# Performance work log

Hardware: AMD Instinct MI355X
Metric: run time of the kernel (lower is better)

## Reference

```python
import jax, jax.numpy as jnp
import numpy as np

B, T, D = 4, 8160, 1024
N, H = 8, 128            # heads, units_per_head (D == N*H)
W = 12                   # block_size
LEFT_CTX = 13            # atten_left_context
L = LEFT_CTX - 1         # left context frames beyond current position
R = 0                    # atten_right_context
C = W + L + R            # context_size = 24
CAP = 50.0               # attention_logits_soft_capping


def _timing_signal(pos, channels):
    # sinusoidal embedding, channels even (1024)
    pos = pos.astype(jnp.float32)
    nt = channels // 2
    inc = np.log(10000.0) / max(nt - 1, 1)
    inv = jnp.exp(jnp.arange(nt, dtype=jnp.float32) * -inc)
    st = pos[:, :, None] * inv[None, None, :]
    return jnp.concatenate([jnp.sin(st), jnp.cos(st)], axis=2)


def _extract_block_context(x, block_size, left, right, pad_val):
    # x: [B, T, ...] -> [B, num_blocks, context_size, ...]
    pads = [(0, 0)] * x.ndim
    pads[1] = (left, right + block_size - 1)
    xp = jnp.pad(x, pads, constant_values=jnp.asarray(pad_val, x.dtype))
    frame_len = block_size + left + right
    num_frames = (xp.shape[1] - frame_len) // block_size + 1
    idx = jnp.arange(num_frames)[:, None] * block_size + jnp.arange(frame_len)[None, :]
    return jnp.take(xp, idx, axis=1)


def _convert_to_block(x, block_size):
    b, t = x.shape[0], x.shape[1]
    nb = t // block_size  # T chosen as multiple of block_size
    return x.reshape((b, nb, block_size) + x.shape[2:])


def setup_inputs() -> dict:
    key = jax.random.key(0)
    ks = jax.random.split(key, 6)
    x = jax.random.normal(ks[0], (B, T, D), dtype=jnp.float32)
    mask = jnp.ones((B, T), dtype=bool)
    i = jnp.arange(W)[:, None]
    j = jnp.arange(C)[None, :]
    causal_valid_mask = (j >= i) & (j - i <= L + R)  # [W, C]
    s = 1.0 / np.sqrt(D)
    wq = jax.random.normal(ks[1], (D, D), dtype=jnp.float32) * s
    wk = jax.random.normal(ks[2], (D, D), dtype=jnp.float32) * s
    wv = jax.random.normal(ks[3], (D, D), dtype=jnp.float32) * s
    pos_proj = jax.random.normal(ks[4], (D, N, H), dtype=jnp.float32) * s
    return {"x": x, "mask": mask, "causal_valid_mask": causal_valid_mask,
            "wq": wq, "wk": wk, "wv": wv, "pos_proj": pos_proj}


def reference(x, mask, causal_valid_mask, wq, wk, wv, pos_proj):
    b, t, d = x.shape
    u = t // W
    q = jnp.einsum('btd,df->btf', x, wq).reshape(b, t, N, H)
    k = jnp.einsum('btd,df->btf', x, wk).reshape(b, t, N, H)
    v = jnp.einsum('btd,df->btf', x, wv).reshape(b, t, N, H)

    q_blk = _convert_to_block(q, W) * (H ** -0.5)        # [B,U,W,N,H]
    k_ctx = _extract_block_context(k, W, L, R, 0.0)      # [B,U,C,N,H]
    v_ctx = _extract_block_context(v, W, L, R, 0.0)      # [B,U,C,N,H]

    # term A+C: content logits
    term_ac = jnp.einsum('BuwNH,BucNH->BNuwc', q_blk, k_ctx)

    # term B+D: relative position logits via skew trick
    pos = jnp.arange(L, -R - 1, -1)[None, :]             # [1, L+R+1]
    sin_emb = _timing_signal(pos, D)                     # [1, L+R+1, D]
    sin_emb = jnp.einsum('fd,dnh->fnh', sin_emb[0], pos_proj)  # [F,N,H]
    term_bd = jnp.einsum('BuwNH,FNH->BNuwF', q_blk, sin_emb)   # [B,N,U,W,F]
    term_bd = jnp.pad(term_bd, ((0, 0),) * 4 + ((0, C + 1 - (L + R + 1)),))
    term_bd = term_bd.reshape(b, N, u, W * (C + 1))[:, :, :, :W * C]
    term_bd = term_bd.reshape(b, N, u, W, C)

    logits = term_ac + term_bd
    logits = CAP * jnp.tanh(logits / CAP)

    mask_ctx = _extract_block_context(mask, W, L, R, False)    # [B,U,C]
    valid = mask_ctx[:, None, :, None, :] & causal_valid_mask[None, None, None, :, :]
    logits = jnp.where(valid, logits, jnp.asarray(-1e9, logits.dtype))
    probs = jax.nn.softmax(logits, axis=-1)              # [B,N,U,W,C]

    out = jnp.einsum('BNuwc,BucNH->BuwNH', probs, v_ctx)
    return out.reshape(b, u * W, N, H)[:, :t]            # [B,T,N,H]
```

## Files before the change

### kernel.cpp

```cpp
#include <hip/hip_runtime.h>
#include <cstdint>
#include <cstddef>


typedef __bf16 bf16_t;
typedef float  floatx4 __attribute__((ext_vector_type(4)));
typedef __bf16 bf16x8  __attribute__((ext_vector_type(8)));
typedef __bf16 bf16x4  __attribute__((ext_vector_type(4)));

#define GLDS16(gp, lp)                                                        \
  __builtin_amdgcn_global_load_lds(                                           \
      (const __attribute__((address_space(1))) void*)(gp),                    \
      (__attribute__((address_space(3))) void*)(lp), 16, 0, 0)

static constexpr int kT     = 8160;
static constexpr int kM     = 4 * kT;
static constexpr int kU     = kT / 12;
static constexpr int kNC    = 3200;
static constexpr size_t kArrE = (size_t)4 * 8 * 8160 * 128;

__global__ __launch_bounds__(256) void convert_x(const float* __restrict__ X,
                                                 bf16_t* __restrict__ Xb) {
  const size_t i = ((size_t)blockIdx.x * 256 + threadIdx.x) * 8;
  float4 a = *(const float4*)(X + i);
  float4 b = *(const float4*)(X + i + 4);
  bf16x8 o;
  o[0] = (bf16_t)a.x; o[1] = (bf16_t)a.y; o[2] = (bf16_t)a.z; o[3] = (bf16_t)a.w;
  o[4] = (bf16_t)b.x; o[5] = (bf16_t)b.y; o[6] = (bf16_t)b.z; o[7] = (bf16_t)b.w;
  *(bf16x8*)(Xb + i) = o;
}

__global__ __launch_bounds__(512) void posemb_k(const float* __restrict__ pp,
                                                float* __restrict__ pe) {
  __shared__ float st[1024];
  __shared__ float red[4][128];
  const int d   = blockIdx.x;
  const int fc  = blockIdx.y;
  const int tid = threadIdx.x;
  const float dpos = (float)d;
  for (int i = tid; i < 1024; i += 512) {
    int idx = i & 511;
    float freq = expf(-(float)idx * (9.2103403719761836f / 511.0f));
    float a = dpos * freq;
    st[i] = (i < 512) ? sinf(a) : cosf(a);
  }
  __syncthreads();
  const int part = tid >> 7;
  const int fl   = tid & 127;
  const int f    = fc * 128 + fl;
  float acc = 0.f;
  const int dd0 = part * 256;
#pragma unroll 8
  for (int dd = dd0; dd < dd0 + 256; ++dd)
    acc += st[dd] * pp[(size_t)dd * 1024 + f];
  red[part][fl] = acc;
  __syncthreads();
  if (tid < 128)
    pe[(size_t)d * 1024 + f] = red[0][fl] + red[1][fl] + red[2][fl] + red[3][fl];
}

__global__ __launch_bounds__(256) void transpose_w(const float* __restrict__ Wq,
                                                   const float* __restrict__ Wk,
                                                   const float* __restrict__ Wv,
                                                   bf16_t* __restrict__ Wt) {
  __shared__ float tile[64][65];
  const int g = blockIdx.z;
  const float* W = (g == 0) ? Wq : (g == 1) ? Wk : Wv;
  bf16_t* O = Wt + (size_t)g * 1024 * 1024;
  const int k0 = blockIdx.x * 64, n0 = blockIdx.y * 64;
  const int col = threadIdx.x & 63, r4 = threadIdx.x >> 6;
#pragma unroll
  for (int i = 0; i < 16; ++i) {
    int row = i * 4 + r4;
    tile[row][col] = W[(size_t)(k0 + row) * 1024 + n0 + col];
  }
  __syncthreads();
#pragma unroll
  for (int i = 0; i < 16; ++i) {
    int row = i * 4 + r4;
    O[(size_t)(n0 + row) * 1024 + k0 + col] = (bf16_t)tile[col][row];
  }
}

__global__ __launch_bounds__(256) void pe2w(const float* __restrict__ pe,
                                            bf16_t* __restrict__ Wt) {
  const int idx = blockIdx.x;
  const int tid = threadIdx.x;
  bf16_t* out = Wt + (size_t)(3072 + idx) * 1024;
  if (idx >= 104) {
    bf16x4 z = {};
    *(bf16x4*)(out + tid * 4) = z;
    return;
  }
  const int n = idx / 13, d = idx - n * 13;
  __shared__ float peh[128];
  if (tid < 128) peh[tid] = pe[(size_t)d * 1024 + n * 128 + tid];
  __syncthreads();
  float acc[4] = {};
  const bf16_t* wb = Wt + (size_t)(n * 128) * 1024 + tid * 4;
#pragma unroll 8
  for (int h = 0; h < 128; ++h) {
    bf16x4 w4 = *(const bf16x4*)(wb + (size_t)h * 1024);
    float s = peh[h];
    acc[0] += s * (float)w4[0];
    acc[1] += s * (float)w4[1];
    acc[2] += s * (float)w4[2];
    acc[3] += s * (float)w4[3];
  }
  bf16x4 o;
  o[0] = (bf16_t)acc[0]; o[1] = (bf16_t)acc[1];
  o[2] = (bf16_t)acc[2]; o[3] = (bf16_t)acc[3];
  *(bf16x4*)(out + tid * 4) = o;
}

__global__ __launch_bounds__(512, 2) void qkv_gemm(const bf16_t* __restrict__ X,
                                                   const bf16_t* __restrict__ Wt,
                                                   bf16_t* __restrict__ O) {
  __shared__ __align__(16) bf16_t lds[8][8192];

  const int flat = blockIdx.x;
  const int work = (flat & 7) * 208 + (flat >> 3);
  const int mt = work / 13, nt = work % 13;
  const int m0 = mt * 256, n0 = nt * 256;

  const int tid  = threadIdx.x;
  const int wave = tid >> 6;
  const int lane = tid & 63;
  const int wm   = wave >> 2;
  const int wn   = wave & 3;
  const int qd   = lane >> 4;
  const int lr   = lane & 15;

  const int rr  = tid >> 3;
  const int cg8 = ((tid & 7) ^ (rr & 7)) * 8;
  const bf16_t* aP[4];
  const bf16_t* bP[4];
  {
    int r2 = m0 + 128 + rr, r3 = m0 + 192 + rr;
    aP[0] = X + (size_t)(m0 + rr) * 1024 + cg8;
    aP[1] = X + (size_t)(m0 + 64 + rr) * 1024 + cg8;
    aP[2] = X + (size_t)(r2 < kM ? r2 : 0) * 1024 + cg8;
    aP[3] = X + (size_t)(r3 < kM ? r3 : 0) * 1024 + cg8;
    int s2 = n0 + 128 + rr, s3 = n0 + 192 + rr;
    bP[0] = Wt + (size_t)(n0 + rr) * 1024 + cg8;
    bP[1] = Wt + (size_t)(n0 + 64 + rr) * 1024 + cg8;
    bP[2] = Wt + (size_t)(s2 < kNC ? s2 : 0) * 1024 + cg8;
    bP[3] = Wt + (size_t)(s3 < kNC ? s3 : 0) * 1024 + cg8;
  }

#define STAGE_A(h, t)                                                          \
  do {                                                                         \
    bf16_t* d_ = &lds[((t) & 1) * 4 + (h)][wave * 512];                        \
    GLDS16(aP[2 * (h)]     + (size_t)(t) * 64, d_);                            \
    GLDS16(aP[2 * (h) + 1] + (size_t)(t) * 64, d_ + 4096);                     \
  } while (0)
#define STAGE_B(h, t)                                                          \
  do {                                                                         \
    bf16_t* d_ = &lds[((t) & 1) * 4 + 2 + (h)][wave * 512];                    \
    GLDS16(bP[2 * (h)]     + (size_t)(t) * 64, d_);                            \
    GLDS16(bP[2 * (h) + 1] + (size_t)(t) * 64, d_ + 4096);                     \
  } while (0)

  auto frag = [&](int slot, int r, int cb) -> bf16x8 {
    uint32_t off = (uint32_t)(r * 128 + cb) ^ (uint32_t)((r & 7) << 4);
    return *(const bf16x8*)((const char*)&lds[slot][0] + off);
  };

  floatx4 acc[8][4] = {};

  STAGE_A(0, 0); STAGE_A(1, 0); STAGE_B(0, 0); STAGE_B(1, 0);
  STAGE_B(0, 1); STAGE_B(1, 1);
  asm volatile("s_waitcnt vmcnt(4)" ::: "memory");
  __builtin_amdgcn_s_barrier();

  const int aslot0 = wm;
  const int bslot0 = 2 + (wn >> 1);
  const int brow0  = (wn & 1) * 64;

#pragma unroll 2
  for (int t = 0; t < 16; ++t) {
    const int par = (t & 1) * 4;
    bf16x8 bfrag[4][2];
#pragma unroll
    for (int p = 0; p < 4; ++p) {
      if (p == 0) {
#pragma unroll
        for (int in = 0; in < 4; ++in)
#pragma unroll
          for (int k2 = 0; k2 < 2; ++k2)
            bfrag[in][k2] =
                frag(par + bslot0, brow0 + in * 16 + lr, k2 * 64 + qd * 16);
      }
      bf16x8 afrag[2][2];
#pragma unroll
      for (int i = 0; i < 2; ++i)
#pragma unroll
        for (int k2 = 0; k2 < 2; ++k2)
          afrag[i][k2] =
              frag(par + aslot0, (2 * p + i) * 16 + lr, k2 * 64 + qd * 16);

      if (p == 0)      { if (t < 15) STAGE_A(0, t + 1); }
      else if (p == 1) { if (t < 15) STAGE_A(1, t + 1); }
      else if (p == 2) { if (t < 14) STAGE_B(0, t + 2); }
      else             { if (t < 14) STAGE_B(1, t + 2); }

      if (p == 3) {
        if (t < 14) asm volatile("s_waitcnt vmcnt(4)" ::: "memory");
        else        asm volatile("s_waitcnt vmcnt(0)" ::: "memory");
      }
      __builtin_amdgcn_s_barrier();
      asm volatile("s_waitcnt lgkmcnt(0)" ::: "memory");
      __builtin_amdgcn_sched_barrier(0);

      __builtin_amdgcn_s_setprio(1);
#pragma unroll
      for (int i = 0; i < 2; ++i)
#pragma unroll
        for (int in = 0; in < 4; ++in)
#pragma unroll
          for (int k2 = 0; k2 < 2; ++k2)
            acc[2 * p + i][in] = __builtin_amdgcn_mfma_f32_16x16x32_bf16(
                afrag[i][k2], bfrag[in][k2], acc[2 * p + i][in], 0, 0, 0);
      __builtin_amdgcn_s_setprio(0);
      __builtin_amdgcn_sched_barrier(0);
      __builtin_amdgcn_s_barrier();
    }
  }
#undef STAGE_A
#undef STAGE_B

  const int mBase = m0 + wm * 128 + qd * 4;
  const int nBase = n0 + wn * 64 + lr;
  bf16_t* QPE = O + 3 * kArrE;
  if (n0 < 3072) {
    const bool interior = (m0 + 256 <= kM);
#pragma unroll
    for (int im = 0; im < 8; ++im)
#pragma unroll
      for (int r = 0; r < 4; ++r) {
        const int mm = mBase + im * 16 + r;
        if (!interior && mm >= kM) continue;
        const int bb = mm / 8160;
        const int tt = mm - bb * 8160;
#pragma unroll
        for (int in = 0; in < 4; ++in) {
          const int nc = nBase + in * 16;
          const int sec = nc >> 10;
          const int nh  = (nc >> 7) & 7;
          const int h   = nc & 127;
          O[(size_t)sec * kArrE +
            (((size_t)(bb * 8 + nh) * 8160 + tt) << 7) + h] =
              (bf16_t)acc[im][in][r];
        }
      }
  } else {
#pragma unroll
    for (int im = 0; im < 8; ++im)
#pragma unroll
      for (int r = 0; r < 4; ++r) {
        const int mm = mBase + im * 16 + r;
        if (mm >= kM) continue;
        const int bb = mm / 8160;
        const int tt = mm - bb * 8160;
#pragma unroll
        for (int in = 0; in < 4; ++in) {
          const int idx = nBase + in * 16 - 3072;
          if (idx < 104) {
            const int nh = idx / 13;
            const int d  = idx - nh * 13;
            QPE[(((size_t)(bb * 8 + nh) * 8160 + tt) << 4) + d] =
                (bf16_t)acc[im][in][r];
          }
        }
      }
  }
}

__global__ __launch_bounds__(256) void qk_soft(const bf16_t* __restrict__ O,
                                               float* __restrict__ Pg) {
  __shared__ __align__(16) bf16_t Ks[80 * 128];
  __shared__ float qpes[64 * 16];

  const int flat  = blockIdx.x;
  const int work  = (flat & 7) * 544 + (flat >> 3);
  const int strip = work >> 5;
  const int rest  = work & 31;
  const int n     = rest >> 2;
  const int b     = rest & 3;
  const int u0    = strip * 5;
  const int t0    = u0 * 12 - 12;
  const int bn    = b * 8 + n;
  const size_t hb = (size_t)bn * kT;
  const int tid  = threadIdx.x;
  const int mi   = tid >> 6;
  const int lane = tid & 63;
  const int qd   = lane >> 4;
  const int lr   = lane & 15;

  const bf16_t* KH  = O + kArrE;
  const bf16_t* QPE = O + 3 * kArrE;

  bf16x8 aQ[4];
  {
    int tq = u0 * 12 + mi * 16 + lr;
    if (tq > kT - 1) tq = kT - 1;
    const bf16_t* qg = O + (hb + tq) * 128;
#pragma unroll
    for (int kk = 0; kk < 4; ++kk)
      aQ[kk] = *(const bf16x8*)(qg + kk * 32 + qd * 8);
  }

  for (int i = tid; i < 80 * 16; i += 256) {
    int row = i >> 4, ch = i & 15;
    int kt = t0 + row;
    bf16x8 k8 = {};
    if (kt >= 0 && kt < kT)
      k8 = *(const bf16x8*)(KH + (hb + kt) * 128 + ch * 8);
    int idx = (row * 128 + ch * 8) ^ ((row & 7) << 3);
    *(bf16x8*)(Ks + idx) = k8;
  }
  if (tid < 120) {
    int m = tid >> 1, hx = tid & 1;
    bf16x8 q8 = *(const bf16x8*)(QPE + (hb + (u0 * 12 + m)) * 16 + hx * 8);
#pragma unroll
    for (int j = 0; j < 8; ++j)
      qpes[m * 16 + hx * 8 + j] = (float)q8[j];
  }
  __syncthreads();

  floatx4 sAcc[2] = {};
#pragma unroll
  for (int ci = 0; ci < 2; ++ci) {
    int krow = (mi + ci) * 16 + lr;
#pragma unroll
    for (int kk = 0; kk < 4; ++kk) {
      int idx = (krow * 128 + kk * 32 + qd * 8) ^ ((krow & 7) << 3);
      bf16x8 bK = *(const bf16x8*)(Ks + idx);
      sAcc[ci] = __builtin_amdgcn_mfma_f32_16x16x32_bf16(aQ[kk], bK, sAcc[ci], 0, 0, 0);
    }
  }

#pragma unroll
  for (int r = 0; r < 4; ++r) {
    const int m = mi * 16 + qd * 4 + r;
    float e[2];
#pragma unroll
    for (int ci = 0; ci < 2; ++ci) {
      int c = (mi + ci) * 16 + lr;
      int d = m + 12 - c;
      int kt = t0 + c;
      bool v = (d >= 0) && (d <= 12) && (kt >= 0) && (m < 60);
      int qidx = m * 16 + (v ? d : 0);
      float s = (sAcc[ci][r] + qpes[qidx]) * 0.0017677669529663689f;
      float t2 = __expf(2.0f * s);
      float th = 1.0f - 2.0f / (t2 + 1.0f);
      e[ci] = v ? __expf(50.0f * th) : 0.0f;
    }
    float sm = e[0] + e[1];
    sm += __shfl_xor(sm, 1);
    sm += __shfl_xor(sm, 2);
    sm += __shfl_xor(sm, 4);
    sm += __shfl_xor(sm, 8);
    float iv = 1.0f / sm;
#pragma unroll
    for (int ci = 0; ci < 2; ++ci) {
      int c = (mi + ci) * 16 + lr;
      int d = m + 12 - c;
      if (m < 60 && d >= 0 && d <= 12)
        Pg[((size_t)bn * kT + (u0 * 12 + m)) * 16 + d] = e[ci] * iv;
    }
  }
}

__global__ __launch_bounds__(256) void pv_k(const bf16_t* __restrict__ O,
                                            const float* __restrict__ Pg,
                                            float* __restrict__ OUT) {
  __shared__ float Vs[60 * 132];
  __shared__ float ps[48 * 16];

  const int flat = blockIdx.x;
  const int work = (flat & 7) * 680 + (flat >> 3);
  const int bn = work / 170, ts = work % 170;
  const int b  = bn >> 3, n = bn & 7;
  const int t1 = ts * 48;
  const size_t hb = (size_t)bn * kT;
  const size_t bbase = (size_t)b * kT;
  const int tid = threadIdx.x;

  const bf16_t* VH = O + 2 * kArrE;

  for (int i = tid; i < 60 * 16; i += 256) {
    int r = i >> 4, ch = i & 15;
    int kt = t1 - 12 + r;
    int vo = r * 132 + ch * 8;
    if (kt < 0) {
      float4 z = {};
      *(float4*)(Vs + vo) = z; *(float4*)(Vs + vo + 4) = z;
    } else {
      bf16x8 v8 = *(const bf16x8*)(VH + (hb + kt) * 128 + ch * 8);
      float4 vl = { (float)v8[0], (float)v8[1], (float)v8[2], (float)v8[3] };
      float4 vh = { (float)v8[4], (float)v8[5], (float)v8[6], (float)v8[7] };
      *(float4*)(Vs + vo) = vl; *(float4*)(Vs + vo + 4) = vh;
    }
  }
  if (tid < 192) {
    int r = tid >> 2, q4 = tid & 3;
    float4 p4 = *(const float4*)(Pg + ((size_t)bn * kT + t1 + r) * 16 + q4 * 4);
    *(float4*)(ps + r * 16 + q4 * 4) = p4;
  }
  __syncthreads();

  for (int i = tid; i < 48 * 32; i += 256) {
    int lt = i >> 5, c4 = i & 31;
    const float* pw = ps + lt * 16;
    float4 acc = {};
#pragma unroll
    for (int d = 0; d <= 12; ++d) {
      float pd = pw[d];
      float4 v4 = *(const float4*)(Vs + (lt + 12 - d) * 132 + c4 * 4);
      acc.x += pd * v4.x; acc.y += pd * v4.y;
      acc.z += pd * v4.z; acc.w += pd * v4.w;
    }
    *(float4*)(OUT + (bbase + t1 + lt) * 1024 + n * 128 + c4 * 4) = acc;
  }
}

extern "C" void kernel_launch(void* const* d_in, const int* in_sizes, int n_in,
                              void* d_out, int out_size, void* d_ws, size_t ws_size,
                              hipStream_t stream) {
  const float* x  = (const float*)d_in[0];
  const float* wq = (const float*)d_in[3];
  const float* wk = (const float*)d_in[4];
  const float* wv = (const float*)d_in[5];
  const float* pp = (const float*)d_in[6];

  char* ws = (char*)d_ws;
  float*  pe  = (float*)ws;
  bf16_t* Wt  = (bf16_t*)(ws + (1u << 16));
  bf16_t* Xb  = (bf16_t*)(ws + (1u << 16) + 8u * 1024 * 1024);
  bf16_t* OH  = (bf16_t*)(ws + (1u << 16) + 8u * 1024 * 1024 +
                          (size_t)kM * 1024 * 2);
  float* Pg = (float*)Xb;
  float* out = (float*)d_out;

  convert_x<<<kM * 1024 / (256 * 8), 256, 0, stream>>>(x, Xb);
  posemb_k<<<dim3(13, 8), 512, 0, stream>>>(pp, pe);
  transpose_w<<<dim3(16, 16, 3), 256, 0, stream>>>(wq, wk, wv, Wt);
  pe2w<<<128, 256, 0, stream>>>(pe, Wt);
  qkv_gemm<<<1664, 512, 0, stream>>>(Xb, Wt, OH);
  qk_soft<<<4352, 256, 0, stream>>>(OH, Pg);
  pv_k<<<5440, 256, 0, stream>>>(OH, Pg, out);
}
```

Before: 584.3 us.

## Fuse QK softmax and PV into a single attention kernel

Merges the logits/softmax kernel and the probability-times-V kernel into one kernel that keeps the probabilities in shared memory and loads the V context per strip. This removes the global write and read of the probability buffer and one kernel launch. In exchange, shared memory per block grows (K tile, fp32 V tile and P tile), which may lower occupancy. K rows beyond 72 are now zeroed rather than loaded.

```diff
diff --git a/kernel.cpp b/kernel.cpp
--- a/kernel.cpp
+++ b/kernel.cpp
@@ -276,10 +276,12 @@
   }
 }
 
-__global__ __launch_bounds__(256) void qk_soft(const bf16_t* __restrict__ O,
-                                               float* __restrict__ Pg) {
+__global__ __launch_bounds__(256) void attn2(const bf16_t* __restrict__ O,
+                                             float* __restrict__ OUT) {
   __shared__ __align__(16) bf16_t Ks[80 * 128];
+  __shared__ float Vs[72 * 132];
   __shared__ float qpes[64 * 16];
+  __shared__ float Ps[60 * 16];
 
   const int flat  = blockIdx.x;
   const int work  = (flat & 7) * 544 + (flat >> 3);
@@ -291,6 +293,7 @@
   const int t0    = u0 * 12 - 12;
   const int bn    = b * 8 + n;
   const size_t hb = (size_t)bn * kT;
+  const size_t bbase = (size_t)b * kT;
   const int tid  = threadIdx.x;
   const int mi   = tid >> 6;
   const int lane = tid & 63;
@@ -298,6 +301,7 @@
   const int lr   = lane & 15;
 
   const bf16_t* KH  = O + kArrE;
+  const bf16_t* VH  = O + 2 * kArrE;
   const bf16_t* QPE = O + 3 * kArrE;
 
   bf16x8 aQ[4];
@@ -314,10 +318,24 @@
     int row = i >> 4, ch = i & 15;
     int kt = t0 + row;
     bf16x8 k8 = {};
-    if (kt >= 0 && kt < kT)
+    if (row < 72 && kt >= 0 && kt < kT)
       k8 = *(const bf16x8*)(KH + (hb + kt) * 128 + ch * 8);
     int idx = (row * 128 + ch * 8) ^ ((row & 7) << 3);
     *(bf16x8*)(Ks + idx) = k8;
+  }
+  for (int i = tid; i < 72 * 16; i += 256) {
+    int row = i >> 4, ch = i & 15;
+    int kt = t0 + row;
+    int vo = row * 132 + ch * 8;
+    if (kt < 0) {
+      float4 z = {};
+      *(float4*)(Vs + vo) = z; *(float4*)(Vs + vo + 4) = z;
+    } else {
+      bf16x8 v8 = *(const bf16x8*)(VH + (hb + kt) * 128 + ch * 8);
+      float4 vl = { (float)v8[0], (float)v8[1], (float)v8[2], (float)v8[3] };
+      float4 vh = { (float)v8[4], (float)v8[5], (float)v8[6], (float)v8[7] };
+      *(float4*)(Vs + vo) = vl; *(float4*)(Vs + vo + 4) = vh;
+    }
   }
   if (tid < 120) {
     int m = tid >> 1, hx = tid & 1;
@@ -367,52 +385,14 @@
       int c = (mi + ci) * 16 + lr;
       int d = m + 12 - c;
       if (m < 60 && d >= 0 && d <= 12)
-        Pg[((size_t)bn * kT + (u0 * 12 + m)) * 16 + d] = e[ci] * iv;
-    }
-  }
-}
-
-__global__ __launch_bounds__(256) void pv_k(const bf16_t* __restrict__ O,
-                                            const float* __restrict__ Pg,
-                                            float* __restrict__ OUT) {
-  __shared__ float Vs[60 * 132];
-  __shared__ float ps[48 * 16];
-
-  const int flat = blockIdx.x;
-  const int work = (flat & 7) * 680 + (flat >> 3);
-  const int bn = work / 170, ts = work % 170;
-  const int b  = bn >> 3, n = bn & 7;
-  const int t1 = ts * 48;
-  const size_t hb = (size_t)bn * kT;
-  const size_t bbase = (size_t)b * kT;
-  const int tid = threadIdx.x;
-
-  const bf16_t* VH = O + 2 * kArrE;
-
-  for (int i = tid; i < 60 * 16; i += 256) {
-    int r = i >> 4, ch = i & 15;
-    int kt = t1 - 12 + r;
-    int vo = r * 132 + ch * 8;
-    if (kt < 0) {
-      float4 z = {};
-      *(float4*)(Vs + vo) = z; *(float4*)(Vs + vo + 4) = z;
-    } else {
-      bf16x8 v8 = *(const bf16x8*)(VH + (hb + kt) * 128 + ch * 8);
-      float4 vl = { (float)v8[0], (float)v8[1], (float)v8[2], (float)v8[3] };
-      float4 vh = { (float)v8[4], (float)v8[5], (float)v8[6], (float)v8[7] };
-      *(float4*)(Vs + vo) = vl; *(float4*)(Vs + vo + 4) = vh;
-    }
-  }
-  if (tid < 192) {
-    int r = tid >> 2, q4 = tid & 3;
-    float4 p4 = *(const float4*)(Pg + ((size_t)bn * kT + t1 + r) * 16 + q4 * 4);
-    *(float4*)(ps + r * 16 + q4 * 4) = p4;
-  }
-  __syncthreads();
-
-  for (int i = tid; i < 48 * 32; i += 256) {
+        Ps[m * 16 + d] = e[ci] * iv;
+    }
+  }
+  __syncthreads();
+
+  for (int i = tid; i < 60 * 32; i += 256) {
     int lt = i >> 5, c4 = i & 31;
-    const float* pw = ps + lt * 16;
+    const float* pw = Ps + lt * 16;
     float4 acc = {};
 #pragma unroll
     for (int d = 0; d <= 12; ++d) {
@@ -421,7 +401,7 @@
       acc.x += pd * v4.x; acc.y += pd * v4.y;
       acc.z += pd * v4.z; acc.w += pd * v4.w;
     }
-    *(float4*)(OUT + (bbase + t1 + lt) * 1024 + n * 128 + c4 * 4) = acc;
+    *(float4*)(OUT + (bbase + u0 * 12 + lt) * 1024 + n * 128 + c4 * 4) = acc;
   }
 }
 
@@ -440,7 +420,6 @@
   bf16_t* Xb  = (bf16_t*)(ws + (1u << 16) + 8u * 1024 * 1024);
   bf16_t* OH  = (bf16_t*)(ws + (1u << 16) + 8u * 1024 * 1024 +
                           (size_t)kM * 1024 * 2);
-  float* Pg = (float*)Xb;
   float* out = (float*)d_out;
 
   convert_x<<<kM * 1024 / (256 * 8), 256, 0, stream>>>(x, Xb);
@@ -448,6 +427,5 @@
   transpose_w<<<dim3(16, 16, 3), 256, 0, stream>>>(wq, wk, wv, Wt);
   pe2w<<<128, 256, 0, stream>>>(pe, Wt);
   qkv_gemm<<<1664, 512, 0, stream>>>(Xb, Wt, OH);
-  qk_soft<<<4352, 256, 0, stream>>>(OH, Pg);
-  pv_k<<<5440, 256, 0, stream>>>(OH, Pg, out);
-}
+  attn2<<<4352, 256, 0, stream>>>(OH, out);
+}
```

Result: slower. 615.5 us (+5.3%).
